# Kernel tuning notes

Measured on AMD Instinct MI355X. Metric: run time of the kernel, lower is better.

The kernel has to match this reference:

```python
import jax, jax.numpy as jnp
import numpy as np

# Multi-scale deformable attention encoder (Mask2Former pixel decoder transformer)
SHAPES = ((64, 64), (32, 32), (16, 16))  # (H, W) per level, strides 8/16/32 of 512x512
HEADS, POINTS, DM = 8, 4, 256
HD = DM // HEADS
NLVL = len(SHAPES)
NLAYERS = 6
STARTS = np.concatenate([[0], np.cumsum([h * w for h, w in SHAPES])])


def layer_norm(x, g, b, eps=1e-5):
    m = x.mean(-1, keepdims=True)
    v = ((x - m) ** 2).mean(-1, keepdims=True)
    return (x - m) * jax.lax.rsqrt(v + eps) * g + b


def ref_points(B, dtype):
    # valid_ratios == 1 (masks are all-False in the module)
    pts = []
    for H, W in SHAPES:
        ys = (jnp.arange(H, dtype=dtype) + 0.5) / H
        xs = (jnp.arange(W, dtype=dtype) + 0.5) / W
        gy, gx = jnp.meshgrid(ys, xs, indexing='ij')
        pts.append(jnp.stack([gx.reshape(-1), gy.reshape(-1)], -1))
    ref = jnp.concatenate(pts, 0)  # [Q,2]
    return jnp.broadcast_to(ref[None, :, None, :], (B, ref.shape[0], NLVL, 2))


def bilinear(value, loc, H, W):
    # grid_sample(align_corners=False, padding_mode='zeros')
    # value: [B,heads,H*W,d]; loc: [B,Q,heads,P,2] normalized to [0,1]
    x = loc[..., 0] * W - 0.5
    y = loc[..., 1] * H - 0.5
    x0f = jnp.floor(x); y0f = jnp.floor(y)
    lx = x - x0f; ly = y - y0f
    x0 = x0f.astype(jnp.int32); y0 = y0f.astype(jnp.int32)
    out = 0.
    for dx, dy, w in ((0, 0, (1 - lx) * (1 - ly)), (1, 0, lx * (1 - ly)),
                      (0, 1, (1 - lx) * ly), (1, 1, lx * ly)):
        xi = x0 + dx; yi = y0 + dy
        valid = (xi >= 0) & (xi < W) & (yi >= 0) & (yi < H)
        idx = jnp.clip(yi, 0, H - 1) * W + jnp.clip(xi, 0, W - 1)  # [B,Q,heads,P]
        idx_t = jnp.transpose(idx, (0, 2, 1, 3))  # [B,heads,Q,P]
        Bq, hq, Qq, Pq = idx_t.shape
        g = jnp.take_along_axis(value, idx_t.reshape(Bq, hq, Qq * Pq, 1), axis=2)
        g = g.reshape(Bq, hq, Qq, Pq, HD)
        wv = (w * valid).transpose(0, 2, 1, 3)[..., None]  # [B,heads,Q,P,1]
        out = out + g * wv
    return out  # [B,heads,Q,P,d]


def msda(query, src, ref, p):
    off_w, off_b, aw_w, aw_b, val_w, val_b, out_w, out_b = p
    B, Q, _ = query.shape
    value = (src @ val_w.T + val_b).reshape(B, Q, HEADS, HD).transpose(0, 2, 1, 3)  # [B,h,Q,d]
    off = (query @ off_w.T + off_b).reshape(B, Q, HEADS, NLVL, POINTS, 2)
    aw = (query @ aw_w.T + aw_b).reshape(B, Q, HEADS, NLVL * POINTS)
    aw = jax.nn.softmax(aw, -1).reshape(B, Q, HEADS, NLVL, POINTS)
    norm = jnp.array([[W, H] for H, W in SHAPES], dtype=query.dtype)  # [L,2] as (W,H)
    loc = ref[:, :, None, :, None, :] + off / norm[None, None, None, :, None, :]
    samp = []
    for l, (H, W) in enumerate(SHAPES):
        v = value[:, :, STARTS[l]:STARTS[l + 1], :]
        samp.append(bilinear(v, loc[:, :, :, l], H, W))  # [B,h,Q,P,d]
    samp = jnp.stack(samp, 3)  # [B,h,Q,L,P,d]
    w = aw.transpose(0, 2, 1, 3, 4)[..., None]  # [B,h,Q,L,P,1]
    o = (samp * w).sum((3, 4)).transpose(0, 2, 1, 3).reshape(B, Q, DM)
    return o @ out_w.T + out_b


def reference(src0, src1, src2, pos0, pos1, pos2, level_embed,
              off_w, off_b, aw_w, aw_b, val_w, val_b, out_w, out_b,
              ln1_g, ln1_b, ffn1_w, ffn1_b, ffn2_w, ffn2_b, ln2_g, ln2_b):
    srcs, poss = [src0, src1, src2], [pos0, pos1, pos2]
    B = src0.shape[0]
    xs, ps = [], []
    for l, (s, pe) in enumerate(zip(srcs, poss)):
        b, c, h, w = s.shape
        xs.append(s.reshape(b, c, h * w).transpose(0, 2, 1))
        ps.append(pe.reshape(b, c, h * w).transpose(0, 2, 1) + level_embed[l])
    x = jnp.concatenate(xs, 1)    # [B,Q,C]
    pos = jnp.concatenate(ps, 1)  # [B,Q,C]
    ref = ref_points(B, x.dtype)
    for i in range(NLAYERS):
        q = x + pos
        attn = msda(q, x, ref, (off_w[i], off_b[i], aw_w[i], aw_b[i],
                                val_w[i], val_b[i], out_w[i], out_b[i]))
        x = layer_norm(x + attn, ln1_g[i], ln1_b[i])
        h = jax.nn.relu(x @ ffn1_w[i].T + ffn1_b[i])
        x = layer_norm(x + h @ ffn2_w[i].T + ffn2_b[i], ln2_g[i], ln2_b[i])
    return x  # memory [B,Q,C]


def setup_inputs() -> dict:
    key = jax.random.key(0)
    ks = jax.random.split(key, 16)
    s = 0.02
    inp = {}
    inp['src0'] = jax.random.normal(ks[0], (4, 256, 64, 64), jnp.float32)
    inp['src1'] = jax.random.normal(ks[1], (4, 256, 32, 32), jnp.float32)
    inp['src2'] = jax.random.normal(ks[2], (4, 256, 16, 16), jnp.float32)
    inp['pos0'] = jax.random.normal(ks[3], (4, 256, 64, 64), jnp.float32)
    inp['pos1'] = jax.random.normal(ks[4], (4, 256, 32, 32), jnp.float32)
    inp['pos2'] = jax.random.normal(ks[5], (4, 256, 16, 16), jnp.float32)
    inp['level_embed'] = jax.random.normal(ks[6], (3, 256), jnp.float32)
    inp['off_w'] = jax.random.normal(ks[7], (6, 192, 256), jnp.float32) * s
    inp['off_b'] = jnp.zeros((6, 192), jnp.float32)
    inp['aw_w'] = jax.random.normal(ks[8], (6, 96, 256), jnp.float32) * s
    inp['aw_b'] = jnp.zeros((6, 96), jnp.float32)
    inp['val_w'] = jax.random.normal(ks[9], (6, 256, 256), jnp.float32) * s
    inp['val_b'] = jnp.zeros((6, 256), jnp.float32)
    inp['out_w'] = jax.random.normal(ks[10], (6, 256, 256), jnp.float32) * s
    inp['out_b'] = jnp.zeros((6, 256), jnp.float32)
    inp['ln1_g'] = jnp.ones((6, 256), jnp.float32)
    inp['ln1_b'] = jnp.zeros((6, 256), jnp.float32)
    inp['ffn1_w'] = jax.random.normal(ks[11], (6, 1024, 256), jnp.float32) * s
    inp['ffn1_b'] = jnp.zeros((6, 1024), jnp.float32)
    inp['ffn2_w'] = jax.random.normal(ks[12], (6, 256, 1024), jnp.float32) * s
    inp['ffn2_b'] = jnp.zeros((6, 256), jnp.float32)
    inp['ln2_g'] = jnp.ones((6, 256), jnp.float32)
    inp['ln2_b'] = jnp.zeros((6, 256), jnp.float32)
    return inp
```

## Files before the change

### kernel.cpp

```cpp
#include <hip/hip_runtime.h>
#include <hip/hip_bf16.h>
#include <math.h>

#define BB 4
#define QTOT 5376
#define DMM 256
#define NHEADS 8
#define HDIM 32
#define NPTS 4
#define NLVLS 3
#define BQ (BB*QTOT)
#define NOA 288

typedef short bf16x8 __attribute__((ext_vector_type(8)));
typedef unsigned short u16x8 __attribute__((ext_vector_type(8)));
typedef float f32x4  __attribute__((ext_vector_type(4)));

__device__ __forceinline__ unsigned short f2b(float f) {
  unsigned int u = __float_as_uint(f);
  unsigned int r = (u + 0x7FFFu + ((u >> 16) & 1u)) >> 16;
  return (unsigned short)r;
}
__device__ __forceinline__ float b2f(unsigned short u) {
  return __uint_as_float(((unsigned int)u) << 16);
}
__device__ __forceinline__ ushort4 f2b4(float4 v) {
  ushort4 o; o.x = f2b(v.x); o.y = f2b(v.y); o.z = f2b(v.z); o.w = f2b(v.w);
  return o;
}

__device__ __forceinline__ void gload16(const void* g, void* l) {
  __builtin_amdgcn_global_load_lds(
      (const __attribute__((address_space(1))) void*)g,
      (__attribute__((address_space(3))) void*)l, 16, 0, 0);
}

__global__ __launch_bounds__(256) void transpose_in(
    const float* __restrict__ src, const float* __restrict__ emb,
    float* __restrict__ dst, int HW, int qstart)
{
  __shared__ float t[32][33];
  int hw0 = blockIdx.x * 32, c0 = blockIdx.y * 32, b = blockIdx.z;
  int tx = threadIdx.x, ty = threadIdx.y;
  const float* s = src + ((size_t)b * DMM + c0) * HW + hw0;
#pragma unroll
  for (int j = 0; j < 4; j++)
    t[ty * 4 + j][tx] = s[(size_t)(ty * 4 + j) * HW + tx];
  __syncthreads();
  float e = emb ? emb[c0 + tx] : 0.0f;
  float* d = dst + ((size_t)b * QTOT + qstart + hw0) * DMM + c0;
#pragma unroll
  for (int j = 0; j < 4; j++)
    d[(size_t)(ty * 4 + j) * DMM + tx] = t[tx][ty * 4 + j] + e;
}

__global__ __launch_bounds__(256) void conv_b(
    const float* __restrict__ s, unsigned short* __restrict__ d, int n4)
{
  int i = blockIdx.x * 256 + threadIdx.x;
  if (i >= n4) return;
  ((ushort4*)d)[i] = f2b4(((const float4*)s)[i]);
}

__global__ __launch_bounds__(256) void pack_oa(
    const float* __restrict__ offw, const float* __restrict__ aww,
    unsigned short* __restrict__ dst)
{
  int i = blockIdx.x * 256 + threadIdx.x;
  if (i >= 6 * NOA * 64) return;
  int c4 = i & 63;
  int row = (i >> 6) % NOA;
  int l = i / (NOA * 64);
  const float* src = (row < 192)
      ? offw + ((size_t)l * 192 + row) * 256
      : aww  + ((size_t)l * 96 + (row - 192)) * 256;
  float4 v = ((const float4*)src)[c4];
  ((ushort4*)dst)[i] = f2b4(v);
}

__global__ __launch_bounds__(256) void pack_oa_bias(
    const float* __restrict__ offb, const float* __restrict__ awb,
    float* __restrict__ dst)
{
  int i = blockIdx.x * 256 + threadIdx.x;
  if (i >= 6 * NOA) return;
  int row = i % NOA, l = i / NOA;
  dst[i] = (row < 192) ? offb[l * 192 + row] : awb[l * 96 + (row - 192)];
}

__global__ __launch_bounds__(256) void prep(
    const float* __restrict__ x, const float* __restrict__ pos,
    unsigned short* __restrict__ xb, unsigned short* __restrict__ qb,
    unsigned short* __restrict__ pos16, int n4)
{
  int i = blockIdx.x * 256 + threadIdx.x;
  if (i >= n4) return;
  float4 a = ((const float4*)x)[i];
  float4 p = ((const float4*)pos)[i];
  ((ushort4*)xb)[i] = f2b4(a);
  ((ushort4*)pos16)[i] = f2b4(p);
  float4 q = make_float4(a.x + p.x, a.y + p.y, a.z + p.z, a.w + p.w);
  ((ushort4*)qb)[i] = f2b4(q);
}

__device__ __forceinline__ void gemm_tile_body(
    const unsigned short* __restrict__ A, const unsigned short* __restrict__ W,
    int m0, int n0, int K,
    unsigned short (*As)[32], unsigned short (*Ws)[32], f32x4 acc[4][4])
{
  int tid = threadIdx.x;
  int wave = tid >> 6, lane = tid & 63;
  int lr = lane & 15;
  int lkr = ((lane >> 4) ^ (lane & 3)) * 8;
  int wrr = (wave >> 1) * 64;
  int wcc = (wave & 1) * 64;

  int srow = lane >> 2;
  int schunk = ((lane & 3) ^ (srow & 3)) * 8;
  const unsigned short* Ag = A + (size_t)(m0 + wave * 32 + srow) * K + schunk;
  const unsigned short* Wg = W + (size_t)(n0 + wave * 32 + srow) * K + schunk;

#define STAGE_BF(k0, buf)                                                      \
  { int bo = (buf) * 128 + wave * 32;                                          \
    gload16(Ag + (k0), &As[bo][0]);                                            \
    gload16(Ag + (size_t)16 * K + (k0), &As[bo + 16][0]);                      \
    gload16(Wg + (k0), &Ws[bo][0]);                                            \
    gload16(Wg + (size_t)16 * K + (k0), &Ws[bo + 16][0]); }

  STAGE_BF(0, 0);
  __syncthreads();
  int cur = 0;
  for (int k0 = 0; k0 < K; k0 += 32) {
    if (k0 + 32 < K) STAGE_BF(k0 + 32, cur ^ 1);
    int bo = cur * 128;
    bf16x8 af[4], bfv[4];
#pragma unroll
    for (int m = 0; m < 4; m++)
      af[m] = *(const bf16x8*)&As[bo + wrr + m * 16 + lr][lkr];
#pragma unroll
    for (int n = 0; n < 4; n++)
      bfv[n] = *(const bf16x8*)&Ws[bo + wcc + n * 16 + lr][lkr];
#pragma unroll
    for (int m = 0; m < 4; m++)
#pragma unroll
      for (int n = 0; n < 4; n++)
        acc[m][n] = __builtin_amdgcn_mfma_f32_16x16x32_bf16(af[m], bfv[n], acc[m][n], 0, 0, 0);
    __syncthreads();
    cur ^= 1;
  }
#undef STAGE_BF
}

__device__ __forceinline__ void gemm_epilogue(
    const float* __restrict__ bias, void* __restrict__ Cout,
    int m0, int n0, int N, int relu, int bfout, f32x4 acc[4][4])
{
  int tid = threadIdx.x;
  int wave = tid >> 6, lane = tid & 63;
  int lr = lane & 15;
  int wrr = (wave >> 1) * 64;
  int wcc = (wave & 1) * 64;
  float* C32 = (float*)Cout;
  unsigned short* C16 = (unsigned short*)Cout;
#pragma unroll
  for (int n = 0; n < 4; n++) {
    int col = n0 + wcc + n * 16 + lr;
    if (col >= N) continue;
    float bv = bias[col];
#pragma unroll
    for (int m = 0; m < 4; m++) {
      int row0 = m0 + wrr + m * 16 + (lane >> 4) * 4;
#pragma unroll
      for (int j = 0; j < 4; j++) {
        float v = acc[m][n][j] + bv;
        if (relu) v = fmaxf(v, 0.0f);
        if (bfout) C16[(size_t)(row0 + j) * N + col] = f2b(v);
        else       C32[(size_t)(row0 + j) * N + col] = v;
      }
    }
  }
}

__global__ __launch_bounds__(256) void gemm_bf(
    const unsigned short* __restrict__ A, const unsigned short* __restrict__ W,
    const float* __restrict__ bias, void* __restrict__ Cout,
    int M, int N, int K, int flags)
{
  __shared__ unsigned short As[256][32];
  __shared__ unsigned short Ws[256][32];
  f32x4 acc[4][4] = {};
  int m0 = blockIdx.x * 128, n0 = blockIdx.y * 128;
  gemm_tile_body(A, W, m0, n0, K, As, Ws, acc);
  gemm_epilogue(bias, Cout, m0, n0, N, flags & 1, flags & 2, acc);
}

__global__ __launch_bounds__(256) void gemm_valoa(
    const unsigned short* __restrict__ xb, const unsigned short* __restrict__ qb,
    const unsigned short* __restrict__ vW, const unsigned short* __restrict__ oaW,
    const float* __restrict__ vBias, const float* __restrict__ oaBias,
    unsigned short* __restrict__ valb16, float* __restrict__ offaw)
{
  __shared__ unsigned short As[256][32];
  __shared__ unsigned short Ws[256][32];
  f32x4 acc[4][4] = {};
  int m0 = blockIdx.x * 128;
  int by = blockIdx.y;
  const int K = 256;
  if (by < 2) {
    int n0 = by * 128;
    gemm_tile_body(xb, vW, m0, n0, K, As, Ws, acc);
    gemm_epilogue(vBias, valb16, m0, n0, 256, 0, 2, acc);
  } else {
    int n0 = (by - 2) * 128;
    gemm_tile_body(qb, oaW, m0, n0, K, As, Ws, acc);
    gemm_epilogue(oaBias, offaw, m0, n0, NOA, 0, 0, acc);
  }
}

__global__ __launch_bounds__(512) void gemm_ln(
    const unsigned short* __restrict__ A, const unsigned short* __restrict__ W,
    const float* __restrict__ bias, const float* __restrict__ g,
    const float* __restrict__ beta, float* __restrict__ x,
    unsigned short* __restrict__ xb, const unsigned short* __restrict__ pos16,
    unsigned short* __restrict__ qb, int K)
{
  __shared__ unsigned short As[64][32];
  __shared__ unsigned short Ws[512][32];

  int m0 = blockIdx.x * 32;
  int tid = threadIdx.x;
  int wave = tid >> 6, lane = tid & 63;
  int lr = lane & 15;
  int lkr = ((lane >> 4) ^ (lane & 3)) * 8;
  int srow = lane >> 2;
  int schunk = ((lane & 3) ^ (srow & 3)) * 8;

  const unsigned short* Ag = A + (size_t)(m0 + (wave & 1) * 16 + srow) * K + schunk;
  const unsigned short* Wg = W + (size_t)(wave * 32 + srow) * K + schunk;

#define STAGE_LN(k0, buf)                                                      \
  { if (wave < 2) gload16(Ag + (k0), &As[(buf) * 32 + wave * 16][0]);          \
    gload16(Wg + (k0),                  &Ws[(buf) * 256 + wave * 32][0]);      \
    gload16(Wg + (size_t)16 * K + (k0), &Ws[(buf) * 256 + wave * 32 + 16][0]); }

  f32x4 acc[2][2] = {};

  STAGE_LN(0, 0);
  __syncthreads();
  int cur = 0;
  for (int k0 = 0; k0 < K; k0 += 32) {
    if (k0 + 32 < K) STAGE_LN(k0 + 32, cur ^ 1);
    bf16x8 af[2], bfv[2];
#pragma unroll
    for (int m = 0; m < 2; m++)
      af[m] = *(const bf16x8*)&As[cur * 32 + m * 16 + lr][lkr];
#pragma unroll
    for (int n = 0; n < 2; n++)
      bfv[n] = *(const bf16x8*)&Ws[cur * 256 + wave * 32 + n * 16 + lr][lkr];
#pragma unroll
    for (int m = 0; m < 2; m++)
#pragma unroll
      for (int n = 0; n < 2; n++)
        acc[m][n] = __builtin_amdgcn_mfma_f32_16x16x32_bf16(af[m], bfv[n], acc[m][n], 0, 0, 0);
    __syncthreads();
    cur ^= 1;
  }
#undef STAGE_LN

#pragma unroll
  for (int n = 0; n < 2; n++) {
    int col = wave * 32 + n * 16 + lr;
    float bv = bias[col];
#pragma unroll
    for (int m = 0; m < 2; m++) {
      int grow = m0 + m * 16 + (lane >> 4) * 4;
#pragma unroll
      for (int j = 0; j < 4; j++)
        acc[m][n][j] += bv + x[(size_t)(grow + j) * DMM + col];
    }
  }

  float2* red = (float2*)&As[0][0];
#pragma unroll
  for (int m = 0; m < 2; m++) {
#pragma unroll
    for (int j = 0; j < 4; j++) {
      float s  = acc[m][0][j] + acc[m][1][j];
      float s2 = acc[m][0][j] * acc[m][0][j] + acc[m][1][j] * acc[m][1][j];
#pragma unroll
      for (int o = 1; o < 16; o <<= 1) {
        s  += __shfl_xor(s,  o, 64);
        s2 += __shfl_xor(s2, o, 64);
      }
      if (lr == 0)
        red[(m * 16 + (lane >> 4) * 4 + j) * 8 + wave] = make_float2(s, s2);
    }
  }
  __syncthreads();

#pragma unroll
  for (int m = 0; m < 2; m++) {
#pragma unroll
    for (int j = 0; j < 4; j++) {
      int rl = m * 16 + (lane >> 4) * 4 + j;
      float ts = 0.f, ts2 = 0.f;
#pragma unroll
      for (int wv = 0; wv < 8; wv++) {
        float2 r = red[rl * 8 + wv];
        ts += r.x; ts2 += r.y;
      }
      float mean = ts * (1.0f / DMM);
      float var  = ts2 * (1.0f / DMM) - mean * mean;
      float sc = rsqrtf(var + 1e-5f);
      int grow = m0 + rl;
#pragma unroll
      for (int n = 0; n < 2; n++) {
        int col = wave * 32 + n * 16 + lr;
        float o = (acc[m][n][j] - mean) * sc * g[col] + beta[col];
        size_t idx = (size_t)grow * DMM + col;
        x[idx]  = o;
        xb[idx] = f2b(o);
        if (qb) qb[idx] = f2b(o + b2f(pos16[idx]));
      }
    }
  }
}

__global__ __launch_bounds__(256) void msda_sample(
    const unsigned short* __restrict__ value, const float* __restrict__ offaw,
    unsigned short* __restrict__ attn16)
{
  __shared__ float saw[8][96];
  __shared__ float smx[64], sinv[64];
  __shared__ float swgt[768 * 4];
  __shared__ int   sofs[768 * 4];

  int tid = threadIdx.x;
  int qi = tid >> 5, t32 = tid & 31;
  int h = t32 >> 2, dg = t32 & 3;
  int bq0 = blockIdx.x * 8;
  int bq = bq0 + qi;
  int b = bq / QTOT;

  for (int i = t32; i < 96; i += 32)
    saw[qi][i] = offaw[(size_t)bq * NOA + 192 + i];
  __syncthreads();

  if (tid < 64) {
    int q2 = tid >> 3, h2 = tid & 7;
    float mx = -1e30f;
#pragma unroll
    for (int t = 0; t < 12; t++) mx = fmaxf(mx, saw[q2][h2 * 12 + t]);
    float den = 0.f;
#pragma unroll
    for (int t = 0; t < 12; t++) den += __expf(saw[q2][h2 * 12 + t] - mx);
    smx[tid] = mx;
    sinv[tid] = 1.0f / den;
  }
  __syncthreads();

  for (int s = tid; s < 768; s += 256) {
    int p = s >> 6;
    int qh = s & 63;
    int q2 = qh >> 3, h2 = qh & 7;
    int l = p >> 2;
    int Wl = 64 >> l;
    int st = (l == 0) ? 0 : ((l == 1) ? 4096 : 5120);

    int q = (bq0 + q2) % QTOT;
    int qq, Wq;
    if (q < 4096)      { qq = q;        Wq = 64; }
    else if (q < 5120) { qq = q - 4096; Wq = 32; }
    else               { qq = q - 5120; Wq = 16; }
    float refx = ((qq % Wq) + 0.5f) / Wq;
    float refy = ((qq / Wq) + 0.5f) / Wq;

    int oi = ((h2 * NLVLS + l) * NPTS + (p & 3)) * 2;
    float2 off2 = *(const float2*)&offaw[(size_t)(bq0 + q2) * NOA + oi];
    float invW = 1.0f / (float)Wl;
    float xf = (refx + off2.x * invW) * Wl - 0.5f;
    float yf = (refy + off2.y * invW) * Wl - 0.5f;
    float x0f = floorf(xf), y0f = floorf(yf);
    float fx = xf - x0f, fy = yf - y0f;
    int x0 = (int)x0f, y0 = (int)y0f;

    float aw = __expf(saw[q2][h2 * 12 + p] - smx[qh]) * sinv[qh];
    float w00 = (1.f - fx) * (1.f - fy) * aw;
    float w10 = fx * (1.f - fy) * aw;
    float w01 = (1.f - fx) * fy * aw;
    float w11 = fx * fy * aw;

    bool xv0 = (x0 >= 0) & (x0 < Wl);
    bool xv1 = (x0 + 1 >= 0) & (x0 + 1 < Wl);
    bool yv0 = (y0 >= 0) & (y0 < Wl);
    bool yv1 = (y0 + 1 >= 0) & (y0 + 1 < Wl);

    int base = s * 4;
    swgt[base + 0] = (xv0 & yv0) ? w00 : 0.f;
    swgt[base + 1] = (xv1 & yv0) ? w10 : 0.f;
    swgt[base + 2] = (xv0 & yv1) ? w01 : 0.f;
    swgt[base + 3] = (xv1 & yv1) ? w11 : 0.f;
    sofs[base + 0] = (xv0 & yv0) ? (st + y0 * Wl + x0) * (DMM * 2) : 0;
    sofs[base + 1] = (xv1 & yv0) ? (st + y0 * Wl + x0 + 1) * (DMM * 2) : 0;
    sofs[base + 2] = (xv0 & yv1) ? (st + (y0 + 1) * Wl + x0) * (DMM * 2) : 0;
    sofs[base + 3] = (xv1 & yv1) ? (st + (y0 + 1) * Wl + x0 + 1) * (DMM * 2) : 0;
  }
  __syncthreads();

  float a8[8];
#pragma unroll
  for (int k = 0; k < 8; k++) a8[k] = 0.f;
  const char* vbase = (const char*)(value + (size_t)b * QTOT * DMM + h * HDIM + dg * 8);
#pragma unroll
  for (int p = 0; p < 12; p++) {
    int s3 = (p * 64 + qi * 8 + h) * 4;
    float4 w = *(const float4*)&swgt[s3];
    int4  of = *(const int4*)&sofs[s3];
    u16x8 g0 = *(const u16x8*)(vbase + of.x);
    u16x8 g1 = *(const u16x8*)(vbase + of.y);
    u16x8 g2 = *(const u16x8*)(vbase + of.z);
    u16x8 g3 = *(const u16x8*)(vbase + of.w);
#pragma unroll
    for (int k = 0; k < 8; k++)
      a8[k] += w.x * b2f((unsigned short)g0[k]) + w.y * b2f((unsigned short)g1[k])
             + w.z * b2f((unsigned short)g2[k]) + w.w * b2f((unsigned short)g3[k]);
  }
  u16x8 o;
#pragma unroll
  for (int k = 0; k < 8; k++) o[k] = f2b(a8[k]);
  *(u16x8*)(attn16 + (size_t)bq * DMM + h * HDIM + dg * 8) = o;
}

extern "C" void kernel_launch(void* const* d_in, const int* in_sizes, int n_in,
                              void* d_out, int out_size, void* d_ws, size_t ws_size,
                              hipStream_t stream)
{
  const float* src[3] = {(const float*)d_in[0], (const float*)d_in[1], (const float*)d_in[2]};
  const float* pin[3] = {(const float*)d_in[3], (const float*)d_in[4], (const float*)d_in[5]};
  const float* lvl_emb = (const float*)d_in[6];
  const float* off_w = (const float*)d_in[7];
  const float* off_b = (const float*)d_in[8];
  const float* aw_w  = (const float*)d_in[9];
  const float* aw_b  = (const float*)d_in[10];
  const float* val_w = (const float*)d_in[11];
  const float* val_b = (const float*)d_in[12];
  const float* out_w = (const float*)d_in[13];
  const float* out_b = (const float*)d_in[14];
  const float* ln1_g = (const float*)d_in[15];
  const float* ln1_b = (const float*)d_in[16];
  const float* ffn1_w = (const float*)d_in[17];
  const float* ffn1_b = (const float*)d_in[18];
  const float* ffn2_w = (const float*)d_in[19];
  const float* ffn2_b = (const float*)d_in[20];
  const float* ln2_g = (const float*)d_in[21];
  const float* ln2_b = (const float*)d_in[22];

  float* x = (float*)d_out;

  char* wsp = (char*)d_ws;
  float* offaw = (float*)wsp;  wsp += (size_t)BQ * NOA * 4;
  unsigned short* valb16 = (unsigned short*)wsp; wsp += (size_t)BQ * 256 * 2;
  unsigned short* attnb  = (unsigned short*)wsp; wsp += (size_t)BQ * 256 * 2;
  unsigned short* hb = (unsigned short*)offaw;
  float* posb = (float*)wsp;  wsp += (size_t)BQ * 256 * 4;
  unsigned short* pos16 = (unsigned short*)wsp; wsp += (size_t)BQ * 256 * 2;
  unsigned short* xb = (unsigned short*)wsp; wsp += (size_t)BQ * 256 * 2;
  unsigned short* qb = (unsigned short*)wsp; wsp += (size_t)BQ * 256 * 2;

  unsigned short* vWb  = (unsigned short*)wsp; wsp += (size_t)6 * 256 * 256 * 2;
  unsigned short* oaWb = (unsigned short*)wsp; wsp += (size_t)6 * NOA * 256 * 2;
  unsigned short* uWb  = (unsigned short*)wsp; wsp += (size_t)6 * 256 * 256 * 2;
  unsigned short* f1Wb = (unsigned short*)wsp; wsp += (size_t)6 * 1024 * 256 * 2;
  unsigned short* f2Wb = (unsigned short*)wsp; wsp += (size_t)6 * 256 * 1024 * 2;
  float* oaBias = (float*)wsp; wsp += (size_t)6 * NOA * 4;
  wsp += 65536;

  conv_b<<<(6 * 65536 / 4 + 255) / 256, 256, 0, stream>>>(val_w, vWb, 6 * 65536 / 4);
  conv_b<<<(6 * 65536 / 4 + 255) / 256, 256, 0, stream>>>(out_w, uWb, 6 * 65536 / 4);
  conv_b<<<(6 * 262144 / 4 + 255) / 256, 256, 0, stream>>>(ffn1_w, f1Wb, 6 * 262144 / 4);
  conv_b<<<(6 * 262144 / 4 + 255) / 256, 256, 0, stream>>>(ffn2_w, f2Wb, 6 * 262144 / 4);
  pack_oa<<<(6 * NOA * 64 + 255) / 256, 256, 0, stream>>>(off_w, aw_w, oaWb);
  pack_oa_bias<<<(6 * NOA + 255) / 256, 256, 0, stream>>>(off_b, aw_b, oaBias);

  const int HWs[3] = {4096, 1024, 256};
  const int starts[3] = {0, 4096, 5120};
  for (int l = 0; l < 3; l++) {
    dim3 g(HWs[l] / 32, DMM / 32, BB), blk(32, 8);
    transpose_in<<<g, blk, 0, stream>>>(src[l], nullptr, x, HWs[l], starts[l]);
    transpose_in<<<g, blk, 0, stream>>>(pin[l], lvl_emb + l * 256, posb, HWs[l], starts[l]);
  }
  prep<<<(BQ * 256 / 4 + 255) / 256, 256, 0, stream>>>(x, posb, xb, qb, pos16, BQ * 256 / 4);

  for (int i = 0; i < 6; i++) {
    gemm_valoa<<<dim3(BQ / 128, 5), 256, 0, stream>>>(
        xb, qb, vWb + (size_t)i * 65536, oaWb + (size_t)i * NOA * 256,
        val_b + i * 256, oaBias + i * NOA, valb16, offaw);
    msda_sample<<<BQ / 8, 256, 0, stream>>>(valb16, offaw, attnb);
    gemm_ln<<<BQ / 32, 512, 0, stream>>>(attnb, uWb + (size_t)i * 65536,
        out_b + i * 256, ln1_g + i * 256, ln1_b + i * 256, x, xb,
        nullptr, nullptr, 256);
    gemm_bf<<<dim3(BQ / 128, 8), 256, 0, stream>>>(xb, f1Wb + (size_t)i * 262144,
        ffn1_b + i * 1024, hb, BQ, 1024, 256, 1 | 2);
    gemm_ln<<<BQ / 32, 512, 0, stream>>>(hb, f2Wb + (size_t)i * 262144,
        ffn2_b + i * 256, ln2_g + i * 256, ln2_b + i * 256, x, xb,
        pos16, qb, 1024);
  }
}
```

Measured before the change: 948.7 us.

## Triple-buffer gemm_ln staging with vmcnt-based waits and balanced load distribution

Replaces the double-buffered LDS pipeline in the GEMM+LayerNorm kernel with a three-stage ring buffer. Global loads are issued two k-steps ahead, and waits use explicit s_waitcnt vmcnt counts instead of a full __syncthreads. The 18 staging slices (A and W) are spread evenly over 6 waves, so the wave that also loads A no longer does extra work. An extra barrier is added before the reduction reuses the As buffer. This costs more shared memory and relies on the hand-set waitcnt values being correct for the async global-to-LDS loads.

```diff
diff --git a/kernel.cpp b/kernel.cpp
--- a/kernel.cpp
+++ b/kernel.cpp
@@ -224,48 +224,88 @@
     unsigned short* __restrict__ xb, const unsigned short* __restrict__ pos16,
     unsigned short* __restrict__ qb, int K)
 {
-  __shared__ unsigned short As[64][32];
-  __shared__ unsigned short Ws[512][32];
+  __shared__ unsigned short As[3][32][32];
+  __shared__ unsigned short Ws[3][256][32];
 
   int m0 = blockIdx.x * 32;
   int tid = threadIdx.x;
   int wave = tid >> 6, lane = tid & 63;
   int lr = lane & 15;
   int lkr = ((lane >> 4) ^ (lane & 3)) * 8;
-  int srow = lane >> 2;
-  int schunk = ((lane & 3) ^ (srow & 3)) * 8;
-
-  const unsigned short* Ag = A + (size_t)(m0 + (wave & 1) * 16 + srow) * K + schunk;
-  const unsigned short* Wg = W + (size_t)(wave * 32 + srow) * K + schunk;
+
+  bool stager = wave < 6;
+  int s0 = wave * 3;
+  int r16 = lane >> 2, cc = lane & 3;
+  int sc8 = (cc ^ (r16 & 3)) * 8;
+  const unsigned short* src0; const unsigned short* src1; const unsigned short* src2;
+  int d0, d1, d2; bool a0, a1, a2;
+  {
+    int s;
+    s = s0;
+    a0 = (s < 2);
+    src0 = a0 ? A + (size_t)(m0 + s * 16 + r16) * K + sc8
+              : W + (size_t)((s - 2) * 16 + r16) * K + sc8;
+    d0 = a0 ? s * 16 : (s - 2) * 16;
+    s = s0 + 1;
+    a1 = (s < 2);
+    src1 = a1 ? A + (size_t)(m0 + s * 16 + r16) * K + sc8
+              : W + (size_t)((s - 2) * 16 + r16) * K + sc8;
+    d1 = a1 ? s * 16 : (s - 2) * 16;
+    s = s0 + 2;
+    a2 = (s < 2);
+    src2 = a2 ? A + (size_t)(m0 + s * 16 + r16) * K + sc8
+              : W + (size_t)((s - 2) * 16 + r16) * K + sc8;
+    d2 = a2 ? s * 16 : (s - 2) * 16;
+  }
 
 #define STAGE_LN(k0, buf)                                                      \
-  { if (wave < 2) gload16(Ag + (k0), &As[(buf) * 32 + wave * 16][0]);          \
-    gload16(Wg + (k0),                  &Ws[(buf) * 256 + wave * 32][0]);      \
-    gload16(Wg + (size_t)16 * K + (k0), &Ws[(buf) * 256 + wave * 32 + 16][0]); }
+  if (stager) {                                                                \
+    gload16(src0 + (k0), a0 ? &As[buf][d0][0] : &Ws[buf][d0][0]);              \
+    gload16(src1 + (k0), a1 ? &As[buf][d1][0] : &Ws[buf][d1][0]);              \
+    gload16(src2 + (k0), a2 ? &As[buf][d2][0] : &Ws[buf][d2][0]);              \
+  }
 
   f32x4 acc[2][2] = {};
 
+#define COMPUTE_LN(buf)                                                        \
+  { bf16x8 af[2], bfv[2];                                                      \
+    _Pragma("unroll")                                                          \
+    for (int m = 0; m < 2; m++)                                                \
+      af[m] = *(const bf16x8*)&As[buf][m * 16 + lr][lkr];                      \
+    _Pragma("unroll")                                                          \
+    for (int n = 0; n < 2; n++)                                                \
+      bfv[n] = *(const bf16x8*)&Ws[buf][wave * 32 + n * 16 + lr][lkr];         \
+    _Pragma("unroll")                                                          \
+    for (int m = 0; m < 2; m++)                                                \
+      _Pragma("unroll")                                                        \
+      for (int n = 0; n < 2; n++)                                              \
+        acc[m][n] = __builtin_amdgcn_mfma_f32_16x16x32_bf16(af[m], bfv[n], acc[m][n], 0, 0, 0); }
+
+  int nst = K >> 5;
   STAGE_LN(0, 0);
-  __syncthreads();
-  int cur = 0;
-  for (int k0 = 0; k0 < K; k0 += 32) {
-    if (k0 + 32 < K) STAGE_LN(k0 + 32, cur ^ 1);
-    bf16x8 af[2], bfv[2];
-#pragma unroll
-    for (int m = 0; m < 2; m++)
-      af[m] = *(const bf16x8*)&As[cur * 32 + m * 16 + lr][lkr];
-#pragma unroll
-    for (int n = 0; n < 2; n++)
-      bfv[n] = *(const bf16x8*)&Ws[cur * 256 + wave * 32 + n * 16 + lr][lkr];
-#pragma unroll
-    for (int m = 0; m < 2; m++)
-#pragma unroll
-      for (int n = 0; n < 2; n++)
-        acc[m][n] = __builtin_amdgcn_mfma_f32_16x16x32_bf16(af[m], bfv[n], acc[m][n], 0, 0, 0);
-    __syncthreads();
-    cur ^= 1;
-  }
+  STAGE_LN(32, 1);
+  asm volatile("s_waitcnt vmcnt(3)" ::: "memory");
+  __builtin_amdgcn_s_barrier();
+  __builtin_amdgcn_sched_barrier(0);
+
+  int bufc = 0;
+  for (int t = 0; t < nst - 2; ++t) {
+    int bufn = bufc + 2; if (bufn >= 3) bufn -= 3;
+    STAGE_LN((size_t)(t + 2) << 5, bufn);
+    COMPUTE_LN(bufc);
+    asm volatile("s_waitcnt vmcnt(3) lgkmcnt(0)" ::: "memory");
+    __builtin_amdgcn_s_barrier();
+    __builtin_amdgcn_sched_barrier(0);
+    if (++bufc == 3) bufc = 0;
+  }
+  COMPUTE_LN(bufc);
+  asm volatile("s_waitcnt vmcnt(0) lgkmcnt(0)" ::: "memory");
+  __builtin_amdgcn_s_barrier();
+  __builtin_amdgcn_sched_barrier(0);
+  if (++bufc == 3) bufc = 0;
+  COMPUTE_LN(bufc);
 #undef STAGE_LN
+#undef COMPUTE_LN
 
 #pragma unroll
   for (int n = 0; n < 2; n++) {
@@ -280,7 +320,8 @@
     }
   }
 
-  float2* red = (float2*)&As[0][0];
+  __syncthreads();
+  float2* red = (float2*)&As[0][0][0];
 #pragma unroll
   for (int m = 0; m < 2; m++) {
 #pragma unroll
```

Measured after the change: 1.017 ms. 1.07x slower.
